# Kernel optimization log

Hardware: AMD Instinct MI355X
Metric: run time of the kernel (lower is better)

Reference implementation:

```python
import jax, jax.numpy as jnp
import numpy as np

EPS = 1.1920929e-07  # torch nn.RMSNorm default eps = finfo(fp32).eps
H, NOPE, ROPE, VD = 16, 128, 64, 128
QKD = NOPE + ROPE


def rmsnorm(x, w):
    return x * jax.lax.rsqrt(jnp.mean(x * x, axis=-1, keepdims=True) + EPS) * w


def rope(x, cos, sin):
    # x: [B,S,h,D]; cos/sin broadcast to [B,S,h,D//2]; pairs are (even, odd) interleaved
    x2 = x.reshape(*x.shape[:-1], -1, 2)
    x0, x1 = x2[..., 0], x2[..., 1]
    r = x0 * cos - x1 * sin
    i = x0 * sin + x1 * cos
    return jnp.stack([r, i], axis=-1).reshape(x.shape)


def setup_inputs() -> dict:
    key = jax.random.key(0)
    ks = jax.random.split(key, 8)
    B, S, D = 2, 2048, 2048
    QR, KR = 1536, 512
    x = jax.random.normal(ks[0], (B, S, D), jnp.float32)
    # RoPE table: theta=10000, rope dim 64 -> 32 frequencies
    pos = np.arange(S)[:, None]
    inv = 1.0 / (10000.0 ** (np.arange(0, ROPE, 2) / ROPE))[None, :]
    ang = pos * inv
    freqs_cos = jnp.asarray(np.cos(ang), jnp.float32)
    freqs_sin = jnp.asarray(np.sin(ang), jnp.float32)

    def w(k, out_dim, in_dim):
        return jax.random.normal(k, (out_dim, in_dim), jnp.float32) / np.sqrt(in_dim)

    return {
        "x": x,
        "freqs_cos": freqs_cos,
        "freqs_sin": freqs_sin,
        "Wq_down": w(ks[1], QR, D),
        "q_norm_w": jnp.ones((QR,), jnp.float32),
        "Wq_up": w(ks[2], H * QKD, QR),
        "Wkv_down": w(ks[3], ROPE + KR, D),
        "kv_norm_w": jnp.ones((KR,), jnp.float32),
        "Wkv_up": w(ks[4], H * (VD + NOPE), KR),
        "Wo": w(ks[5], D, H * VD),
        "bo": jnp.zeros((D,), jnp.float32),
        "start_pos": 0,
    }


def reference(x, freqs_cos, freqs_sin, Wq_down, q_norm_w, Wq_up, Wkv_down, kv_norm_w, Wkv_up, Wo, bo, start_pos):
    B, S, D = x.shape
    cos = freqs_cos[None, :, None, :]
    sin = freqs_sin[None, :, None, :]
    # low-rank Q path: down -> RMSNorm -> up
    q = rmsnorm(x @ Wq_down.T, q_norm_w) @ Wq_up.T
    q = q.reshape(B, S, H, QKD)
    q_nope, q_rope = q[..., :NOPE], q[..., NOPE:]
    q_rope = rope(q_rope, cos, sin)
    q = jnp.concatenate([q_nope, q_rope], axis=-1)  # [B,S,H,QKD]
    # low-rank KV path: shared rope part + latent kv
    kv = x @ Wkv_down.T
    k_rope, c_kv = kv[..., :ROPE], kv[..., ROPE:]
    k_rope = rope(k_rope[:, :, None, :], cos, sin)  # [B,S,1,ROPE]
    kv = rmsnorm(c_kv, kv_norm_w) @ Wkv_up.T
    kv = kv.reshape(B, S, H, NOPE + VD)
    k_nope, v = kv[..., :NOPE], kv[..., NOPE:]
    k = jnp.concatenate([k_nope, jnp.broadcast_to(k_rope, (B, S, H, ROPE))], axis=-1)
    # causal SDPA (start_pos=0 prefill: cache slice equals fresh K/V)
    scale = 1.0 / np.sqrt(QKD)
    scores = jnp.einsum("bqhd,bkhd->bhqk", q, k) * scale
    mask = jnp.tril(jnp.ones((S, S), bool))
    scores = jnp.where(mask, scores, -jnp.inf)
    attn = jax.nn.softmax(scores, axis=-1)
    o = jnp.einsum("bhqk,bkhd->bqhd", attn, v).reshape(B, S, H * VD)
    return o @ Wo.T + bo
```

## Files before the change

kernel.cpp:

```cpp
#include <hip/hip_runtime.h>
#include <hip/hip_bf16.h>
#include <stdint.h>


typedef short bf16x8 __attribute__((ext_vector_type(8)));
typedef float f32x4  __attribute__((ext_vector_type(4)));
typedef unsigned int u32;

#define RMS_EPS 1.1920929e-07f
#define SCALE_L2E 0.10411931095f

__device__ __forceinline__ unsigned short f2b(float f) {
  union { float f; uint32_t u; } c; c.f = f;
  uint32_t u = c.u;
  return (unsigned short)((u + 0x7FFFu + ((u >> 16) & 1u)) >> 16);
}
__device__ __forceinline__ float b2f(short s) {
  union { uint32_t u; float f; } c; c.u = ((uint32_t)(unsigned short)s) << 16;
  return c.f;
}
__device__ __forceinline__ u32 pk2(float a, float b) {
  union { __hip_bfloat162 h; u32 u; } cv;
  cv.h = __float22bfloat162_rn(float2{a, b});
  return cv.u;
}
__device__ __forceinline__ void gld16(const short* g, short* l) {
  __builtin_amdgcn_global_load_lds(
      (const __attribute__((address_space(1))) u32*)g,
      (__attribute__((address_space(3))) u32*)l, 16, 0, 0);
}

__device__ __forceinline__ void cvt4(const float* __restrict__ in,
                                     short* __restrict__ out, int i) {
  float4 v = ((const float4*)in)[i];
  union { ushort4 s; uint2 u; } o;
  o.s.x = f2b(v.x); o.s.y = f2b(v.y); o.s.z = f2b(v.z); o.s.w = f2b(v.w);
  ((uint2*)out)[i] = o.u;
}

__global__ void f2bf_all_kernel(
    const float* __restrict__ x,    short* __restrict__ x_bf,
    const float* __restrict__ Wqd,  short* __restrict__ w_qd,
    const float* __restrict__ Wqu,  short* __restrict__ w_qu,
    const float* __restrict__ Wkvu, short* __restrict__ w_kvu,
    const float* __restrict__ Wo,   short* __restrict__ w_o,
    const float* __restrict__ Wkvd, short* __restrict__ w_kvd) {
  int i = blockIdx.x * 256 + threadIdx.x;
  if (i < 2097152) { cvt4(x, x_bf, i); return; }
  i -= 2097152;
  if (i < 786432) { cvt4(Wqd, w_qd, i); return; }
  i -= 786432;
  if (i < 1179648) { cvt4(Wqu, w_qu, i); return; }
  i -= 1179648;
  if (i < 524288) { cvt4(Wkvu, w_kvu, i); return; }
  i -= 524288;
  if (i < 1048576) { cvt4(Wo, w_o, i); return; }
  i -= 1048576;
  if (i >= 327680) return;
  int row = i >> 9;
  ushort4 s = {0, 0, 0, 0};
  if (row < 576) {
    float4 v = ((const float4*)Wkvd)[i];
    s.x = f2b(v.x); s.y = f2b(v.y); s.z = f2b(v.z); s.w = f2b(v.w);
  }
  union { ushort4 ss; uint2 u; } o; o.ss = s;
  ((uint2*)w_kvd)[i] = o.u;
}

template <int EPI>
__global__ __launch_bounds__(256) void gemm_bt(
    const short* __restrict__ A, const short* __restrict__ Bt,
    void* __restrict__ Cv, const float* __restrict__ bias,
    int K, int ldc,
    const float* __restrict__ fc, const float* __restrict__ fs,
    short* __restrict__ aux) {
  __shared__ __align__(16) short As[128 * 32];
  __shared__ __align__(16) short Bs[128 * 32];
  int nx = gridDim.x;
  int lin = blockIdx.y * nx + blockIdx.x;
  int cpx = (nx * gridDim.y) >> 3;
  int swz = (lin & 7) * cpx + (lin >> 3);
  int row0 = (swz / nx) * 128, col0 = (swz % nx) * 128;
  int t = threadIdx.x, lane = t & 63, w = t >> 6;
  int wm = w >> 1, wn = w & 1;
  int l15 = lane & 15, l4 = lane >> 4;
  f32x4 acc[4][4] = {};

  int srow = lane >> 2, scol = (lane & 3) * 8;
  const short* Ag = A + (size_t)(row0 + srow) * K + scol;
  const short* Bg = Bt + (size_t)(col0 + srow) * K + scol;

  for (int kt = 0; kt < K; kt += 32) {
#pragma unroll
    for (int c = 0; c < 2; ++c) {
      int blk = w * 2 + c;
      gld16(Ag + (size_t)(blk * 16) * K + kt, As + blk * 512);
      gld16(Bg + (size_t)(blk * 16) * K + kt, Bs + blk * 512);
    }
    __syncthreads();
    bf16x8 af[4], bfr[4];
#pragma unroll
    for (int i = 0; i < 4; ++i) {
      af[i]  = *(const bf16x8*)(As + (wm * 64 + i * 16 + l15) * 32 + l4 * 8);
      bfr[i] = *(const bf16x8*)(Bs + (wn * 64 + i * 16 + l15) * 32 + l4 * 8);
    }
#pragma unroll
    for (int i = 0; i < 4; ++i)
#pragma unroll
      for (int j = 0; j < 4; ++j)
        acc[i][j] = __builtin_amdgcn_mfma_f32_16x16x32_bf16(af[i], bfr[j], acc[i][j], 0, 0, 0);
    __syncthreads();
  }

  if constexpr (EPI == 0) {
    float* C = (float*)Cv;
#pragma unroll
    for (int j = 0; j < 4; ++j) {
      int col = col0 + wn * 64 + j * 16 + l15;
      float bv = bias ? bias[col] : 0.0f;
#pragma unroll
      for (int i = 0; i < 4; ++i) {
        int row = row0 + wm * 64 + i * 16 + l4 * 4;
        float* dst = C + (size_t)row * ldc + col;
#pragma unroll
        for (int r = 0; r < 4; ++r) dst[(size_t)r * ldc] = acc[i][j][r] + bv;
      }
    }
  } else if constexpr (EPI == 1) {
    short* C = (short*)Cv;
#pragma unroll
    for (int j = 0; j < 4; ++j) {
      int col = col0 + wn * 64 + j * 16 + l15;
#pragma unroll
      for (int i = 0; i < 4; ++i) {
        int row = row0 + wm * 64 + i * 16 + l4 * 4;
        short* dst = C + (size_t)row * ldc + col;
#pragma unroll
        for (int r = 0; r < 4; ++r) dst[(size_t)r * ldc] = (short)f2b(acc[i][j][r]);
      }
    }
  } else if constexpr (EPI == 2) {
    short* qb = (short*)Cv;
#pragma unroll
    for (int j = 0; j < 4; ++j) {
      int col = col0 + wn * 64 + j * 16 + l15;
      int h = col / 192;
      int d = col - h * 192;
      bool ro = (d >= 128);
      int ir = ro ? ((d - 128) >> 1) : 0;
      bool odd = (l15 & 1);
#pragma unroll
      for (int i = 0; i < 4; ++i) {
        int rowb = row0 + wm * 64 + i * 16 + l4 * 4;
#pragma unroll
        for (int r = 0; r < 4; ++r) {
          int row = rowb + r;
          int b = row >> 11, s = row & 2047;
          float v = acc[i][j][r];
          float pv = __shfl_xor(v, 1);
          float o;
          if (ro) {
            float c = fc[s * 32 + ir], sn = fs[s * 32 + ir];
            o = odd ? (pv * sn + v * c) : (v * c - pv * sn);
          } else {
            o = v;
          }
          qb[((size_t)((b * 16 + h) * 2048 + s)) * 192 + d] = (short)f2b(o * SCALE_L2E);
        }
      }
    }
  } else {
    short* kb = (short*)Cv;
    short* vT = aux;
    int h = col0 >> 8;
    if ((col0 & 128) == 0) {
#pragma unroll
      for (int j = 0; j < 4; ++j) {
        int d = wn * 64 + j * 16 + l15;
#pragma unroll
        for (int i = 0; i < 4; ++i) {
          int rowb = row0 + wm * 64 + i * 16 + l4 * 4;
#pragma unroll
          for (int r = 0; r < 4; ++r) {
            int row = rowb + r;
            int b = row >> 11, s = row & 2047;
            kb[((size_t)((b * 16 + h) * 2048 + s)) * 128 + d] = (short)f2b(acc[i][j][r]);
          }
        }
      }
    } else {
#pragma unroll
      for (int j = 0; j < 4; ++j) {
        int dv = wn * 64 + j * 16 + l15;
#pragma unroll
        for (int i = 0; i < 4; ++i) {
          int s0 = row0 + wm * 64 + i * 16 + l4 * 4;
          int b = s0 >> 11, s = s0 & 2047;
          short4 o;
          o.x = (short)f2b(acc[i][j][0]);
          o.y = (short)f2b(acc[i][j][1]);
          o.z = (short)f2b(acc[i][j][2]);
          o.w = (short)f2b(acc[i][j][3]);
          *(short4*)(vT + ((size_t)((b * 16 + h) * 128 + dv)) * 2048 + s) = o;
        }
      }
    }
  }
}

template <int W>
__global__ __launch_bounds__(256) void rmsnorm_wave(
    const short* __restrict__ in, const float* __restrict__ wgt,
    short* __restrict__ out, int ld_in) {
  constexpr int NC = W / 512;
  int row = blockIdx.x * 4 + (threadIdx.x >> 6);
  int lane = threadIdx.x & 63;
  const short* x = in + (size_t)row * ld_in + lane * 8;
  float vals[NC * 8];
  float ss = 0.f;
#pragma unroll
  for (int c = 0; c < NC; ++c) {
    bf16x8 v = *(const bf16x8*)(x + c * 512);
#pragma unroll
    for (int k = 0; k < 8; ++k) {
      float f = b2f(v[k]);
      vals[c * 8 + k] = f; ss += f * f;
    }
  }
#pragma unroll
  for (int off = 32; off > 0; off >>= 1) ss += __shfl_xor(ss, off);
  float rs = rsqrtf(ss / (float)W + RMS_EPS);
  short* o = out + (size_t)row * W + lane * 8;
#pragma unroll
  for (int c = 0; c < NC; ++c) {
    const float4* wp = (const float4*)(wgt + c * 512 + lane * 8);
    float4 w0 = wp[0], w1 = wp[1];
    ushort4 lo, hi;
    lo.x = f2b(vals[c * 8 + 0] * rs * w0.x);
    lo.y = f2b(vals[c * 8 + 1] * rs * w0.y);
    lo.z = f2b(vals[c * 8 + 2] * rs * w0.z);
    lo.w = f2b(vals[c * 8 + 3] * rs * w0.w);
    hi.x = f2b(vals[c * 8 + 4] * rs * w1.x);
    hi.y = f2b(vals[c * 8 + 5] * rs * w1.y);
    hi.z = f2b(vals[c * 8 + 6] * rs * w1.z);
    hi.w = f2b(vals[c * 8 + 7] * rs * w1.w);
    *(ushort4*)(o + c * 512) = lo;
    *(ushort4*)(o + c * 512 + 4) = hi;
  }
}

__global__ void prep_krope_kernel(const short* __restrict__ c1,
                                  const float* __restrict__ fc,
                                  const float* __restrict__ fs,
                                  short* __restrict__ kr) {
  int idx = blockIdx.x * 256 + threadIdx.x;
  int i = idx & 31;
  int s = (idx >> 5) & 2047;
  int b = idx >> 16;
  const short* row = c1 + (size_t)(b * 2048 + s) * 2176 + 1536 + 2 * i;
  float x0 = b2f(row[0]), x1 = b2f(row[1]);
  float c = fc[s * 32 + i], sn = fs[s * 32 + i];
  uint32_t pk = (uint32_t)f2b(x0 * c - x1 * sn) | ((uint32_t)f2b(x0 * sn + x1 * c) << 16);
  *(uint32_t*)(kr + ((size_t)(b * 2048 + s)) * 64 + 2 * i) = pk;
}

__global__ __launch_bounds__(256) void attn_kernel(
    const short* __restrict__ qb, const short* __restrict__ kb,
    const short* __restrict__ kr, const short* __restrict__ vtb,
    short* __restrict__ ob) {
  __shared__ __align__(16) short Ks[64 * 196];
  __shared__ __align__(16) short Vs[128 * 70];
  int bid = blockIdx.x;
  int xcd = bid & 7, kk2 = bid >> 3;
  int bh = xcd * 4 + (kk2 >> 4);
  int qx = kk2 & 15;
  int b = bh >> 4, h = bh & 15;
  int t = threadIdx.x, lane = t & 63, w = t >> 6;
  int l15 = lane & 15, l4 = lane >> 4;
  const short* Kbh = kb + (size_t)bh * 2048 * 128;
  const short* krb = kr + (size_t)b * 2048 * 64;
  const short* Vbh = vtb + (size_t)bh * 128 * 2048;

  int kn_r = t >> 4, kn_c = (t & 15) * 8;
  int kr_r = t >> 3, kr_c = (t & 7) * 8;
  int v_d = t >> 3, v_c = (t & 7) * 8;

  int sA = (l15 + ((l4 & 1) << 5)) << 2;
  int sB = sA + (16 << 2);
  bool chi = (l4 >> 1) != 0;

  for (int half = 0; half < 2; ++half) {
    int qt = half ? (31 - qx) : qx;
    int q0 = qt * 64;
    const short* Qbase = qb + ((size_t)bh * 2048 + q0 + w * 16) * 192;
    bf16x8 qf[6];
#pragma unroll
    for (int kk = 0; kk < 6; ++kk)
      qf[kk] = *(const bf16x8*)(Qbase + (size_t)l15 * 192 + kk * 32 + l4 * 8);
    f32x4 oaccT[8] = {};
    float m_i = -1e30f, l_i = 0.f;
    int qcol = q0 + w * 16 + l15;
    int kend = q0 + 64;

    for (int kt = 0; kt < kend; kt += 64) {
#pragma unroll
      for (int c = 0; c < 4; ++c) {
        int r = kn_r + 16 * c;
        *(bf16x8*)(Ks + r * 196 + kn_c) =
            *(const bf16x8*)(Kbh + (size_t)(kt + r) * 128 + kn_c);
      }
#pragma unroll
      for (int c = 0; c < 2; ++c) {
        int r = kr_r + 32 * c;
        *(bf16x8*)(Ks + r * 196 + 128 + kr_c) =
            *(const bf16x8*)(krb + (size_t)(kt + r) * 64 + kr_c);
      }
#pragma unroll
      for (int c = 0; c < 4; ++c) {
        int d = v_d + 32 * c;
        *(bf16x8*)(Vs + d * 70 + v_c) =
            *(const bf16x8*)(Vbh + (size_t)d * 2048 + kt + v_c);
      }
      __syncthreads();

      f32x4 s[4] = {};
      __builtin_amdgcn_s_setprio(1);
#pragma unroll
      for (int kk = 0; kk < 6; ++kk) {
#pragma unroll
        for (int c = 0; c < 4; ++c) {
          bf16x8 kf = *(const bf16x8*)(Ks + (c * 16 + l15) * 196 + kk * 32 + l4 * 8);
          s[c] = __builtin_amdgcn_mfma_f32_16x16x32_bf16(kf, qf[kk], s[c], 0, 0, 0);
        }
      }
      __builtin_amdgcn_s_setprio(0);

      if (kt == q0) {
#pragma unroll
        for (int c = 0; c < 4; ++c)
#pragma unroll
          for (int r = 0; r < 4; ++r) {
            int k = kt + c * 16 + l4 * 4 + r;
            if (k > qcol) s[c][r] = -1e30f;
          }
      }
      float mx = fmaxf(fmaxf(fmaxf(s[0][0], s[0][1]), fmaxf(s[0][2], s[0][3])),
                       fmaxf(fmaxf(s[1][0], s[1][1]), fmaxf(s[1][2], s[1][3])));
      mx = fmaxf(mx, fmaxf(fmaxf(fmaxf(s[2][0], s[2][1]), fmaxf(s[2][2], s[2][3])),
                           fmaxf(fmaxf(s[3][0], s[3][1]), fmaxf(s[3][2], s[3][3]))));
      mx = fmaxf(mx, __shfl_xor(mx, 16));
      mx = fmaxf(mx, __shfl_xor(mx, 32));
      float newm = fmaxf(m_i, mx);
      float alpha = __builtin_amdgcn_exp2f(m_i - newm);
      float rs = 0.f;
#pragma unroll
      for (int c = 0; c < 4; ++c)
#pragma unroll
        for (int r = 0; r < 4; ++r) {
          float p = __builtin_amdgcn_exp2f(s[c][r] - newm);
          s[c][r] = p; rs += p;
        }
      rs += __shfl_xor(rs, 16);
      rs += __shfl_xor(rs, 32);
      l_i = l_i * alpha + rs;
      m_i = newm;
#pragma unroll
      for (int dt = 0; dt < 8; ++dt)
#pragma unroll
        for (int r = 0; r < 4; ++r) oaccT[dt][r] *= alpha;

      u32 pk00 = pk2(s[0][0], s[0][1]), pk01 = pk2(s[0][2], s[0][3]);
      u32 pk10 = pk2(s[1][0], s[1][1]), pk11 = pk2(s[1][2], s[1][3]);
      u32 pk20 = pk2(s[2][0], s[2][1]), pk21 = pk2(s[2][2], s[2][3]);
      u32 pk30 = pk2(s[3][0], s[3][1]), pk31 = pk2(s[3][2], s[3][3]);
      union { bf16x8 v; u32 u[4]; } P0, P1;
      {
        u32 a0 = __builtin_amdgcn_ds_bpermute(sA, (int)pk00);
        u32 a1 = __builtin_amdgcn_ds_bpermute(sA, (int)pk01);
        u32 a2 = __builtin_amdgcn_ds_bpermute(sB, (int)pk00);
        u32 a3 = __builtin_amdgcn_ds_bpermute(sB, (int)pk01);
        u32 b0 = __builtin_amdgcn_ds_bpermute(sA, (int)pk10);
        u32 b1 = __builtin_amdgcn_ds_bpermute(sA, (int)pk11);
        u32 b2 = __builtin_amdgcn_ds_bpermute(sB, (int)pk10);
        u32 b3 = __builtin_amdgcn_ds_bpermute(sB, (int)pk11);
        P0.u[0] = chi ? b0 : a0; P0.u[1] = chi ? b1 : a1;
        P0.u[2] = chi ? b2 : a2; P0.u[3] = chi ? b3 : a3;
      }
      {
        u32 a0 = __builtin_amdgcn_ds_bpermute(sA, (int)pk20);
        u32 a1 = __builtin_amdgcn_ds_bpermute(sA, (int)pk21);
        u32 a2 = __builtin_amdgcn_ds_bpermute(sB, (int)pk20);
        u32 a3 = __builtin_amdgcn_ds_bpermute(sB, (int)pk21);
        u32 b0 = __builtin_amdgcn_ds_bpermute(sA, (int)pk30);
        u32 b1 = __builtin_amdgcn_ds_bpermute(sA, (int)pk31);
        u32 b2 = __builtin_amdgcn_ds_bpermute(sB, (int)pk30);
        u32 b3 = __builtin_amdgcn_ds_bpermute(sB, (int)pk31);
        P1.u[0] = chi ? b0 : a0; P1.u[1] = chi ? b1 : a1;
        P1.u[2] = chi ? b2 : a2; P1.u[3] = chi ? b3 : a3;
      }

      __builtin_amdgcn_s_setprio(1);
#pragma unroll
      for (int dt = 0; dt < 8; ++dt) {
        bf16x8 vf0 = *(const bf16x8*)(Vs + (dt * 16 + l15) * 70 + l4 * 8);
        bf16x8 vf1 = *(const bf16x8*)(Vs + (dt * 16 + l15) * 70 + 32 + l4 * 8);
        oaccT[dt] = __builtin_amdgcn_mfma_f32_16x16x32_bf16(vf0, P0.v, oaccT[dt], 0, 0, 0);
        oaccT[dt] = __builtin_amdgcn_mfma_f32_16x16x32_bf16(vf1, P1.v, oaccT[dt], 0, 0, 0);
      }
      __builtin_amdgcn_s_setprio(0);
      __syncthreads();
    }
    float inv = 1.0f / l_i;
    short* dst = ob + ((size_t)(b * 2048 + qcol)) * 2048 + h * 128;
#pragma unroll
    for (int dt = 0; dt < 8; ++dt) {
      uint2 o;
      o.x = pk2(oaccT[dt][0] * inv, oaccT[dt][1] * inv);
      o.y = pk2(oaccT[dt][2] * inv, oaccT[dt][3] * inv);
      *(uint2*)(dst + dt * 16 + l4 * 4) = o;
    }
  }
}

extern "C" void kernel_launch(void* const* d_in, const int* in_sizes, int n_in,
                              void* d_out, int out_size, void* d_ws, size_t ws_size,
                              hipStream_t stream) {
  const float* x    = (const float*)d_in[0];
  const float* fcos = (const float*)d_in[1];
  const float* fsin = (const float*)d_in[2];
  const float* Wqd  = (const float*)d_in[3];
  const float* qnw  = (const float*)d_in[4];
  const float* Wqu  = (const float*)d_in[5];
  const float* Wkvd = (const float*)d_in[6];
  const float* kvnw = (const float*)d_in[7];
  const float* Wkvu = (const float*)d_in[8];
  const float* Wo   = (const float*)d_in[9];
  const float* bo   = (const float*)d_in[10];
  float* out = (float*)d_out;
  char* ws = (char*)d_ws;

  short* x_bf  = (short*)(ws + 0);
  short* w_cat = (short*)(ws + 16777216);
  short* w_qu  = (short*)(ws + 25690112);
  short* w_kvu = (short*)(ws + 35127296);
  short* w_o   = (short*)(ws + 39321600);
  short* c1    = (short*)(ws + 47710208);
  short* qn    = (short*)(ws + 65536000);
  short* ckvn  = (short*)(ws + 78118912);
  short* q_b   = (short*)(ws + 82313216);
  short* k_b   = (short*)(ws + 107479040);
  short* vT    = (short*)(ws + 132644864);
  short* o_bf  = (short*)(ws + 149422080);
  short* kr    = (short*)(ws + 166199296);

  f2bf_all_kernel<<<23296, 256, 0, stream>>>(x, x_bf, Wqd, w_cat, Wqu, w_qu,
                                             Wkvu, w_kvu, Wo, w_o,
                                             Wkvd, w_cat + 1536 * 2048);

  gemm_bt<1><<<dim3(17, 32), 256, 0, stream>>>(x_bf, w_cat, c1, nullptr, 2048, 2176,
                                               nullptr, nullptr, nullptr);
  prep_krope_kernel<<<512, 256, 0, stream>>>(c1, fcos, fsin, kr);
  rmsnorm_wave<1536><<<1024, 256, 0, stream>>>(c1, qnw, qn, 2176);
  rmsnorm_wave<512><<<1024, 256, 0, stream>>>(c1 + 1600, kvnw, ckvn, 2176);

  gemm_bt<2><<<dim3(24, 32), 256, 0, stream>>>(qn, w_qu, q_b, nullptr, 1536, 0,
                                               fcos, fsin, nullptr);
  gemm_bt<3><<<dim3(32, 32), 256, 0, stream>>>(ckvn, w_kvu, k_b, nullptr, 512, 0,
                                               nullptr, nullptr, vT);

  attn_kernel<<<512, 256, 0, stream>>>(q_b, k_b, kr, vT, o_bf);

  gemm_bt<0><<<dim3(16, 32), 256, 0, stream>>>(o_bf, w_o, out, bo, 2048, 2048,
                                               nullptr, nullptr, nullptr);
}
```

Baseline: 354.4 us.

## Swap MFMA operands for row-contiguous vector epilogue stores; fuse norm/krope kernels

For the non-V GEMM epilogues, the MFMA operands are swapped so each lane holds four consecutive columns of one row. That lets the f32 output, bf16 c1 and the RoPE'd Q be written with vectorized float4/uint2 stores, and the RoPE pair is handled in-register instead of with a cross-lane shuffle. The two RMSNorm launches and the k-rope prep launch are merged into one kernel that dispatches on block index, saving two launches. The risk is extra divergence in the fused kernel.

```diff
diff --git a/kernel.cpp b/kernel.cpp
--- a/kernel.cpp
+++ b/kernel.cpp
@@ -107,66 +107,72 @@
 #pragma unroll
     for (int i = 0; i < 4; ++i)
 #pragma unroll
-      for (int j = 0; j < 4; ++j)
-        acc[i][j] = __builtin_amdgcn_mfma_f32_16x16x32_bf16(af[i], bfr[j], acc[i][j], 0, 0, 0);
+      for (int j = 0; j < 4; ++j) {
+        if constexpr (EPI == 3)
+          acc[i][j] = __builtin_amdgcn_mfma_f32_16x16x32_bf16(af[i], bfr[j], acc[i][j], 0, 0, 0);
+        else
+          acc[i][j] = __builtin_amdgcn_mfma_f32_16x16x32_bf16(bfr[j], af[i], acc[i][j], 0, 0, 0);
+      }
     __syncthreads();
   }
 
   if constexpr (EPI == 0) {
     float* C = (float*)Cv;
 #pragma unroll
-    for (int j = 0; j < 4; ++j) {
-      int col = col0 + wn * 64 + j * 16 + l15;
-      float bv = bias ? bias[col] : 0.0f;
-#pragma unroll
-      for (int i = 0; i < 4; ++i) {
-        int row = row0 + wm * 64 + i * 16 + l4 * 4;
-        float* dst = C + (size_t)row * ldc + col;
-#pragma unroll
-        for (int r = 0; r < 4; ++r) dst[(size_t)r * ldc] = acc[i][j][r] + bv;
+    for (int i = 0; i < 4; ++i) {
+      int row = row0 + wm * 64 + i * 16 + l15;
+#pragma unroll
+      for (int j = 0; j < 4; ++j) {
+        int coln = col0 + wn * 64 + j * 16 + l4 * 4;
+        float4 bv = {0.f, 0.f, 0.f, 0.f};
+        if (bias) bv = *(const float4*)(bias + coln);
+        float4 o;
+        o.x = acc[i][j][0] + bv.x; o.y = acc[i][j][1] + bv.y;
+        o.z = acc[i][j][2] + bv.z; o.w = acc[i][j][3] + bv.w;
+        *(float4*)(C + (size_t)row * ldc + coln) = o;
       }
     }
   } else if constexpr (EPI == 1) {
     short* C = (short*)Cv;
 #pragma unroll
-    for (int j = 0; j < 4; ++j) {
-      int col = col0 + wn * 64 + j * 16 + l15;
-#pragma unroll
-      for (int i = 0; i < 4; ++i) {
-        int row = row0 + wm * 64 + i * 16 + l4 * 4;
-        short* dst = C + (size_t)row * ldc + col;
-#pragma unroll
-        for (int r = 0; r < 4; ++r) dst[(size_t)r * ldc] = (short)f2b(acc[i][j][r]);
+    for (int i = 0; i < 4; ++i) {
+      int row = row0 + wm * 64 + i * 16 + l15;
+#pragma unroll
+      for (int j = 0; j < 4; ++j) {
+        int coln = col0 + wn * 64 + j * 16 + l4 * 4;
+        uint2 o;
+        o.x = pk2(acc[i][j][0], acc[i][j][1]);
+        o.y = pk2(acc[i][j][2], acc[i][j][3]);
+        *(uint2*)(C + (size_t)row * ldc + coln) = o;
       }
     }
   } else if constexpr (EPI == 2) {
     short* qb = (short*)Cv;
 #pragma unroll
-    for (int j = 0; j < 4; ++j) {
-      int col = col0 + wn * 64 + j * 16 + l15;
-      int h = col / 192;
-      int d = col - h * 192;
-      bool ro = (d >= 128);
-      int ir = ro ? ((d - 128) >> 1) : 0;
-      bool odd = (l15 & 1);
-#pragma unroll
-      for (int i = 0; i < 4; ++i) {
-        int rowb = row0 + wm * 64 + i * 16 + l4 * 4;
-#pragma unroll
-        for (int r = 0; r < 4; ++r) {
-          int row = rowb + r;
-          int b = row >> 11, s = row & 2047;
-          float v = acc[i][j][r];
-          float pv = __shfl_xor(v, 1);
-          float o;
-          if (ro) {
-            float c = fc[s * 32 + ir], sn = fs[s * 32 + ir];
-            o = odd ? (pv * sn + v * c) : (v * c - pv * sn);
-          } else {
-            o = v;
-          }
-          qb[((size_t)((b * 16 + h) * 2048 + s)) * 192 + d] = (short)f2b(o * SCALE_L2E);
+    for (int i = 0; i < 4; ++i) {
+      int row = row0 + wm * 64 + i * 16 + l15;
+      int b = row >> 11, s = row & 2047;
+#pragma unroll
+      for (int j = 0; j < 4; ++j) {
+        int coln = col0 + wn * 64 + j * 16 + l4 * 4;
+        int h = coln / 192;
+        int d0 = coln - h * 192;
+        float v0 = acc[i][j][0], v1 = acc[i][j][1];
+        float v2 = acc[i][j][2], v3 = acc[i][j][3];
+        float o0, o1, o2, o3;
+        if (d0 >= 128) {
+          int ir0 = (d0 - 128) >> 1;
+          float c0 = fc[s * 32 + ir0], s0 = fs[s * 32 + ir0];
+          float c1 = fc[s * 32 + ir0 + 1], s1 = fs[s * 32 + ir0 + 1];
+          o0 = v0 * c0 - v1 * s0; o1 = v0 * s0 + v1 * c0;
+          o2 = v2 * c1 - v3 * s1; o3 = v2 * s1 + v3 * c1;
+        } else {
+          o0 = v0; o1 = v1; o2 = v2; o3 = v3;
         }
+        uint2 o;
+        o.x = pk2(o0 * SCALE_L2E, o1 * SCALE_L2E);
+        o.y = pk2(o2 * SCALE_L2E, o3 * SCALE_L2E);
+        *(uint2*)(qb + ((size_t)((b * 16 + h) * 2048 + s)) * 192 + d0) = o;
       }
     }
   } else {
@@ -209,11 +215,11 @@
 }
 
 template <int W>
-__global__ __launch_bounds__(256) void rmsnorm_wave(
+__device__ __forceinline__ void rms_body(
     const short* __restrict__ in, const float* __restrict__ wgt,
-    short* __restrict__ out, int ld_in) {
+    short* __restrict__ out, int ld_in, int blk) {
   constexpr int NC = W / 512;
-  int row = blockIdx.x * 4 + (threadIdx.x >> 6);
+  int row = blk * 4 + (threadIdx.x >> 6);
   int lane = threadIdx.x & 63;
   const short* x = in + (size_t)row * ld_in + lane * 8;
   float vals[NC * 8];
@@ -249,19 +255,28 @@
   }
 }
 
-__global__ void prep_krope_kernel(const short* __restrict__ c1,
-                                  const float* __restrict__ fc,
-                                  const float* __restrict__ fs,
-                                  short* __restrict__ kr) {
-  int idx = blockIdx.x * 256 + threadIdx.x;
-  int i = idx & 31;
-  int s = (idx >> 5) & 2047;
-  int b = idx >> 16;
-  const short* row = c1 + (size_t)(b * 2048 + s) * 2176 + 1536 + 2 * i;
-  float x0 = b2f(row[0]), x1 = b2f(row[1]);
-  float c = fc[s * 32 + i], sn = fs[s * 32 + i];
-  uint32_t pk = (uint32_t)f2b(x0 * c - x1 * sn) | ((uint32_t)f2b(x0 * sn + x1 * c) << 16);
-  *(uint32_t*)(kr + ((size_t)(b * 2048 + s)) * 64 + 2 * i) = pk;
+__global__ __launch_bounds__(256) void norm_krope_kernel(
+    const short* __restrict__ c1,
+    const float* __restrict__ qnw, short* __restrict__ qn,
+    const float* __restrict__ kvnw, short* __restrict__ ckvn,
+    const float* __restrict__ fc, const float* __restrict__ fs,
+    short* __restrict__ kr) {
+  int bb = blockIdx.x;
+  if (bb < 1024) {
+    rms_body<1536>(c1, qnw, qn, 2176, bb);
+  } else if (bb < 2048) {
+    rms_body<512>(c1 + 1600, kvnw, ckvn, 2176, bb - 1024);
+  } else {
+    int idx = (bb - 2048) * 256 + threadIdx.x;
+    int i = idx & 31;
+    int s = (idx >> 5) & 2047;
+    int b = idx >> 16;
+    const short* row = c1 + (size_t)(b * 2048 + s) * 2176 + 1536 + 2 * i;
+    float x0 = b2f(row[0]), x1 = b2f(row[1]);
+    float c = fc[s * 32 + i], sn = fs[s * 32 + i];
+    uint32_t pk = (uint32_t)f2b(x0 * c - x1 * sn) | ((uint32_t)f2b(x0 * sn + x1 * c) << 16);
+    *(uint32_t*)(kr + ((size_t)(b * 2048 + s)) * 64 + 2 * i) = pk;
+  }
 }
 
 __global__ __launch_bounds__(256) void attn_kernel(
@@ -459,9 +474,8 @@
 
   gemm_bt<1><<<dim3(17, 32), 256, 0, stream>>>(x_bf, w_cat, c1, nullptr, 2048, 2176,
                                                nullptr, nullptr, nullptr);
-  prep_krope_kernel<<<512, 256, 0, stream>>>(c1, fcos, fsin, kr);
-  rmsnorm_wave<1536><<<1024, 256, 0, stream>>>(c1, qnw, qn, 2176);
-  rmsnorm_wave<512><<<1024, 256, 0, stream>>>(c1 + 1600, kvnw, ckvn, 2176);
+  norm_krope_kernel<<<2560, 256, 0, stream>>>(c1, qnw, qn, kvnw, ckvn,
+                                              fcos, fsin, kr);
 
   gemm_bt<2><<<dim3(24, 32), 256, 0, stream>>>(qn, w_qu, q_b, nullptr, 1536, 0,
                                                fcos, fsin, nullptr);
```

After: 356.8 us. About the same (+0.7%).
